# Optimization experiments

Hardware: AMD Instinct MI355X
Metric: run time of the kernel (lower is better)

## Reference

```python
import jax, jax.numpy as jnp
import numpy as np

B, N, DIM = 8, 1024, 768
HEADS, HEAD_DIM = 8, 96
EXPERTS, TASKS = 24, 9
SCALE = HEAD_DIM ** -0.5
SWITCHLOSS_W, ZLOSS_W = 0.1, 0.001


def setup_inputs() -> dict:
    key = jax.random.key(0)
    ks = jax.random.split(key, 6)
    x = jax.random.normal(ks[0], (B, N, DIM), jnp.float32)
    Wg = jax.random.normal(ks[1], (TASKS, DIM, EXPERTS), jnp.float32) * 0.02  # per-task gate
    W1 = jax.random.normal(ks[2], (EXPERTS, DIM, HEAD_DIM), jnp.float32) * 0.02  # experts (map)
    W2 = jax.random.normal(ks[3], (EXPERTS, HEAD_DIM, DIM), jnp.float32) * 0.02  # output_experts (reduce)
    Wkv = jax.random.normal(ks[4], (DIM, 2 * HEAD_DIM), jnp.float32) * 0.02      # shared kv proj
    b_kv = jax.random.normal(ks[5], (2 * HEAD_DIM,), jnp.float32) * 0.02
    return {"x": x, "Wg\u200b".replace("\u200b", ""): Wg, "W1": W1, "W2": W2, "Wkv": Wkv, "b_kv": b_kv, "task_bh": 3}


def reference(x, Wg, W1, W2, Wkv, b_kv, task_bh):
    # ---- TaskMoE top-k gating (eval mode: clean logits, no noise/sampling) ----
    logits = jnp.einsum('bnd,de->bne', x, Wg[task_bh])            # [B,N,E]
    probs = jax.nn.softmax(logits, axis=-1)
    top_g, top_i = jax.lax.top_k(probs, HEADS)                    # [B,N,H]
    denom = jax.lax.stop_gradient(jnp.sum(top_g, -1, keepdims=True) + 1e-6)
    gates = top_g / denom                                         # normalized top-k gates

    # ---- aux losses: switch (load-balance) + z-loss (cvloss weight is 0) ----
    me = probs.reshape(-1, EXPERTS).sum(0)
    me = me / me.sum()
    freqs = jnp.zeros((EXPERTS,), x.dtype).at[top_i.reshape(-1)].add(1.0)
    fe = freqs / freqs.sum()
    switch_loss = EXPERTS * jnp.sum(me * fe)
    z_loss = jnp.mean(jax.nn.logsumexp(logits.reshape(-1, EXPERTS), axis=-1) ** 2)
    aux_loss = SWITCHLOSS_W * switch_loss + ZLOSS_W * z_loss

    # ---- MoE map: per-head q from selected experts (dense compute + gather) ----
    all_q = jnp.einsum('bnd,edh->bneh', x, W1)                    # [B,N,E,Hd]
    q = jnp.take_along_axis(all_q, top_i[..., None], axis=2)      # [B,N,H,Hd]

    # ---- shared-KV multi-head attention ----
    kv = x @ Wkv + b_kv
    k, v = jnp.split(kv, 2, axis=-1)                              # [B,N,Hd] each
    attn = jnp.einsum('bihd,bjd->bhij', q, k) * SCALE             # [B,H,N,N]
    attn = jax.nn.softmax(attn, axis=-1)
    o = jnp.einsum('bhij,bjd->bihd', attn, v)                     # [B,N,H,Hd]

    # ---- MoE reduce: gate-weighted combine through output experts ----
    comb = jax.nn.one_hot(top_i, EXPERTS, dtype=x.dtype) * gates[..., None]  # [B,N,H,E]
    mixed = jnp.einsum('bnhe,bnhd->bned', comb, o)                # [B,N,E,Hd]
    out = jnp.einsum('bned,edc->bnc', mixed, W2)                  # [B,N,DIM]
    return out, aux_loss
```

## Files before the change

### kernel.cpp

```cpp
#include <hip/hip_runtime.h>
#include <hip/hip_bf16.h>
#include <stdint.h>

#define DEVFN static __device__ __forceinline__

typedef __attribute__((ext_vector_type(8))) short bf16x8;
typedef __attribute__((ext_vector_type(4))) short s16x4;
typedef __attribute__((ext_vector_type(4))) float f32x4;

static constexpr int TOK = 8192;
static constexpr int DIM = 768;
static constexpr int HEADS = 8;
static constexpr int HD = 96;
static constexpr int EXPERTS = 24;
static constexpr int NQ = 2304;
static constexpr int NQP = 2560;
static constexpr float C2 = 0.14724484f;
static constexpr float THRRAW = 78.0f;

static constexpr size_t OFF_XB   = 0;
static constexpr size_t OFF_BT1  = 12582912;
static constexpr size_t OFF_W2T  = 16515072;
static constexpr size_t OFF_K    = 20054016;
static constexpr size_t OFF_VT   = 21626880;
static constexpr size_t OFF_GATE = 23199744;
static constexpr size_t OFF_TOPI = 23461888;
static constexpr size_t OFF_AUX  = 23724032;
static constexpr size_t OFF_ALLQ = 23724288;
static constexpr size_t OFF_PART = OFF_ALLQ;
static constexpr size_t OFF_LOGT = OFF_ALLQ + 12582912;

DEVFN short f2bf(float f){
  __hip_bfloat16 h = __float2bfloat16(f);
  return __builtin_bit_cast(short, h);
}
DEVFN float bf2f(short u){
  return __bfloat162float(__builtin_bit_cast(__hip_bfloat16, u));
}

DEVFN void gload16(const void* g, void* l){
  auto gp = reinterpret_cast<__attribute__((address_space(1))) unsigned int*>(
      reinterpret_cast<uintptr_t>(g));
  auto lp = reinterpret_cast<__attribute__((address_space(3))) unsigned int*>(
      reinterpret_cast<uintptr_t>(l));
  __builtin_amdgcn_global_load_lds(gp, lp, 16, 0, 0);
}

__global__ __launch_bounds__(256) void prep_kernel(const float* __restrict__ W1,
                                                   const float* __restrict__ Wkv,
                                                   const float* __restrict__ W2,
                                                   short* __restrict__ Bt1,
                                                   short* __restrict__ W2t){
  __shared__ float tl[6240];
  int bid = blockIdx.x, tid = threadIdx.x;

  if (bid < 288){
    int e = bid / 12, dt = bid - e*12;
    int d0 = dt*64;
    const float* src = W1 + (size_t)e*(DIM*HD);
#pragma unroll
    for (int it = 0; it < 6; ++it){
      int c = it*256 + tid;
      int row = c / 24, q = c - row*24;
      float4 v = *reinterpret_cast<const float4*>(src + (size_t)(d0+row)*HD + q*4);
      float* dst = &tl[row*97 + q*4];
      dst[0]=v.x; dst[1]=v.y; dst[2]=v.z; dst[3]=v.w;
    }
    __syncthreads();
#pragma unroll
    for (int it = 0; it < 6; ++it){
      int c = it*256 + tid;
      int hh = c >> 4, cq = c & 15;
      s16x4 o4;
#pragma unroll
      for (int j = 0; j < 4; ++j) o4[j] = f2bf(tl[(cq*4+j)*97 + hh]);
      *reinterpret_cast<s16x4*>(Bt1 + (size_t)(e*HD + hh)*DIM + d0 + cq*4) = o4;
    }
  } else if (bid < 312){
    int t = bid - 288;
    int jb = t / 12, dt = t - jb*12;
    int j0 = jb*96, d0 = dt*64;
#pragma unroll
    for (int it = 0; it < 6; ++it){
      int c = it*256 + tid;
      int row = c / 24, q = c - row*24;
      float4 v = *reinterpret_cast<const float4*>(Wkv + (size_t)(d0+row)*192 + j0 + q*4);
      float* dst = &tl[row*97 + q*4];
      dst[0]=v.x; dst[1]=v.y; dst[2]=v.z; dst[3]=v.w;
    }
    __syncthreads();
#pragma unroll
    for (int it = 0; it < 6; ++it){
      int c = it*256 + tid;
      int jj = c >> 4, cq = c & 15;
      s16x4 o4;
#pragma unroll
      for (int j = 0; j < 4; ++j) o4[j] = f2bf(tl[(cq*4+j)*97 + jj]);
      *reinterpret_cast<s16x4*>(Bt1 + (size_t)(NQ + j0 + jj)*DIM + d0 + cq*4) = o4;
    }
  } else if (bid < 600){
    int t = bid - 312;
    int e = t / 12, ct = t - e*12;
    int c0 = ct*64;
    const float* src = W2 + (size_t)e*(HD*DIM);
#pragma unroll
    for (int it = 0; it < 6; ++it){
      int c = it*256 + tid;
      int hh = c >> 4, q = c & 15;
      float4 v = *reinterpret_cast<const float4*>(src + (size_t)hh*DIM + c0 + q*4);
      float* dst = &tl[hh*65 + q*4];
      dst[0]=v.x; dst[1]=v.y; dst[2]=v.z; dst[3]=v.w;
    }
    __syncthreads();
#pragma unroll
    for (int it = 0; it < 6; ++it){
      int c = it*256 + tid;
      int cr = c / 24, q = c - cr*24;
      s16x4 o4;
#pragma unroll
      for (int j = 0; j < 4; ++j) o4[j] = f2bf(tl[(q*4+j)*65 + cr]);
      *reinterpret_cast<s16x4*>(W2t + (size_t)(c0 + cr)*NQ + e*HD + q*4) = o4;
    }
  } else {
    int i = (bid-600)*256 + tid;
    Bt1[(size_t)(NQ + 192)*DIM + i] = 0;
  }
}

__global__ __launch_bounds__(64) void gating_partial(const float* __restrict__ x,
                                                     const float* __restrict__ Wg,
                                                     const int* __restrict__ task,
                                                     short* __restrict__ xb,
                                                     float* __restrict__ partial){
  __shared__ float xl[64*49];
  int lane = threadIdx.x;
  int tg = blockIdx.x >> 4, kc = blockIdx.x & 15;
  int tok0 = tg*64, kbase = kc*48;
  const float* Wt = Wg + (size_t)task[0]*(DIM*EXPERTS) + (size_t)kbase*EXPERTS;

#pragma unroll
  for (int i = 0; i < 12; ++i){
    int c = i*64 + lane;
    int t = c / 12, cc = c - t*12;
    size_t gidx = (size_t)(tok0+t)*DIM + kbase + cc*4;
    float4 v = *reinterpret_cast<const float4*>(x + gidx);
    float* dst = &xl[t*49 + cc*4];
    dst[0] = v.x; dst[1] = v.y; dst[2] = v.z; dst[3] = v.w;
    s16x4 o4;
    o4[0] = f2bf(v.x); o4[1] = f2bf(v.y); o4[2] = f2bf(v.z); o4[3] = f2bf(v.w);
    *reinterpret_cast<s16x4*>(xb + gidx) = o4;
  }
  __syncthreads();

  float acc[EXPERTS];
#pragma unroll
  for (int e = 0; e < EXPERTS; ++e) acc[e] = 0.f;
  for (int d = 0; d < 48; ++d){
    float xv = xl[lane*49 + d];
    const float* wr = Wt + d*EXPERTS;
#pragma unroll
    for (int e = 0; e < EXPERTS; ++e) acc[e] = fmaf(xv, wr[e], acc[e]);
  }
#pragma unroll
  for (int e = 0; e < EXPERTS; ++e)
    partial[(size_t)(kc*EXPERTS + e)*TOK + tok0 + lane] = acc[e];
}

__global__ __launch_bounds__(256) void gating_combine(const float* __restrict__ partial,
                                                      float* __restrict__ logT){
  int idx = blockIdx.x*256 + threadIdx.x;
  float s = 0.f;
#pragma unroll
  for (int kc = 0; kc < 16; ++kc)
    s += partial[(size_t)kc*EXPERTS*TOK + idx];
  logT[idx] = s;
}

__global__ __launch_bounds__(256) void gating_select(const float* __restrict__ logT,
                                                     int* __restrict__ topi,
                                                     float* __restrict__ gates,
                                                     float* __restrict__ auxbuf){
  __shared__ float lme[EXPERTS];
  __shared__ float lfr[EXPERTS];
  __shared__ float lz;
  int tid = threadIdx.x;
  int lane = tid & 63;
  int token = blockIdx.x*256 + tid;
  if (tid < EXPERTS){ lme[tid] = 0.f; lfr[tid] = 0.f; }
  if (tid == 0) lz = 0.f;
  __syncthreads();

  float acc[EXPERTS];
#pragma unroll
  for (int e = 0; e < EXPERTS; ++e)
    acc[e] = logT[(size_t)e*TOK + token];

  float mx = acc[0];
#pragma unroll
  for (int e = 1; e < EXPERTS; ++e) mx = fmaxf(mx, acc[e]);
  unsigned selm = 0; int sel[8]; float sg[8];
#pragma unroll
  for (int t = 0; t < 8; ++t){
    float best = -3.0e38f; int bi = 0;
#pragma unroll
    for (int e = 0; e < EXPERTS; ++e){
      bool ok = !((selm>>e)&1u) && (acc[e] > best);
      best = ok ? acc[e] : best;
      bi   = ok ? e      : bi;
    }
    selm |= (1u<<bi); sel[t] = bi; sg[t] = best;
  }

  float p[EXPERTS]; float S = 0.f;
#pragma unroll
  for (int e = 0; e < EXPERTS; ++e){ p[e] = __expf(acc[e] - mx); S += p[e]; }
  float lse = mx + __logf(S);
  float Sinv = 1.f/S;
  float gsum = 0.f; float pg[8];
#pragma unroll
  for (int t = 0; t < 8; ++t){ pg[t] = __expf(sg[t] - mx)*Sinv; gsum += pg[t]; }
  float dinv = 1.f/(gsum + 1e-6f);

#pragma unroll
  for (int t = 0; t < 8; ++t){
    topi[token*HEADS + t]  = sel[t];
    gates[token*HEADS + t] = pg[t]*dinv;
  }

  float z2 = lse*lse;
#pragma unroll
  for (int d = 1; d < 64; d <<= 1) z2 += __shfl_xor(z2, d, 64);
#pragma unroll
  for (int e = 0; e < EXPERTS; ++e){
    float v = p[e]*Sinv;
#pragma unroll
    for (int d = 1; d < 64; d <<= 1) v += __shfl_xor(v, d, 64);
    bool hit = (sel[0]==e)|(sel[1]==e)|(sel[2]==e)|(sel[3]==e)|
               (sel[4]==e)|(sel[5]==e)|(sel[6]==e)|(sel[7]==e);
    unsigned long long bal = __ballot(hit);
    if (lane == 0){
      atomicAdd(&lme[e], v);
      atomicAdd(&lfr[e], (float)__popcll(bal));
    }
  }
  if (lane == 0) atomicAdd(&lz, z2);
  __syncthreads();
  if (tid < EXPERTS){
    atomicAdd(&auxbuf[tid], lme[tid]);
    atomicAdd(&auxbuf[EXPERTS + tid], lfr[tid]);
  } else if (tid == 63) atomicAdd(&auxbuf[2*EXPERTS], lz);
}

__global__ void aux_final(const float* __restrict__ auxbuf, float* __restrict__ outa){
  if (threadIdx.x != 0 || blockIdx.x != 0) return;
  float ms = 0.f, fs = 0.f;
  for (int e=0;e<EXPERTS;++e){ ms += auxbuf[e]; fs += auxbuf[EXPERTS+e]; }
  float sw = 0.f;
  for (int e=0;e<EXPERTS;++e) sw += (auxbuf[e]/ms)*(auxbuf[EXPERTS+e]/fs);
  sw *= (float)EXPERTS;
  float z = auxbuf[2*EXPERTS] / (float)TOK;
  outa[0] = 0.1f*sw + 0.001f*z;
}

template<bool OUT_BF16>
__global__ __launch_bounds__(256) void gemm_bt(const short* __restrict__ A,
                                               const short* __restrict__ Bt,
                                               void* __restrict__ Cout,
                                               int M, int N, int K){
  __shared__ short As[128*64];
  __shared__ short Bs[128*64];
  int nwg = gridDim.x*gridDim.y;
  int orig = blockIdx.y*gridDim.x + blockIdx.x;
  int cpx = nwg >> 3;
  int swz = (orig & 7)*cpx + (orig >> 3);
  int bx = swz % gridDim.x, by = swz / gridDim.x;

  int tid = threadIdx.x;
  int lane = tid & 63, w = tid >> 6;
  int wr = w >> 1, wc = w & 1;
  int l15 = lane & 15, lg = lane >> 4;
  int m0 = by * 128, n0 = bx * 128;

  f32x4 acc[4][4] = {};

  for (int k0 = 0; k0 < K; k0 += 64){
#pragma unroll
    for (int it = 0; it < 4; ++it){
      int c = it*256 + tid;
      int row = c >> 3, cc = c & 7;
      int csrc = cc ^ (row & 7);
      gload16(A  + (size_t)(m0+row)*K + k0 + csrc*8, (char*)As + (size_t)c*16);
      gload16(Bt + (size_t)(n0+row)*K + k0 + csrc*8, (char*)Bs + (size_t)c*16);
    }
    __syncthreads();
#pragma unroll
    for (int kk = 0; kk < 2; ++kk){
      bf16x8 af[4], bfr[4];
      int jp = (kk*4 + lg) ^ (l15 & 7);
#pragma unroll
      for (int m = 0; m < 4; ++m)
        af[m] = *reinterpret_cast<const bf16x8*>(&As[(wr*64 + m*16 + l15)*64 + jp*8]);
#pragma unroll
      for (int n = 0; n < 4; ++n)
        bfr[n] = *reinterpret_cast<const bf16x8*>(&Bs[(wc*64 + n*16 + l15)*64 + jp*8]);
#pragma unroll
      for (int m = 0; m < 4; ++m)
#pragma unroll
        for (int n = 0; n < 4; ++n)
          acc[m][n] = __builtin_amdgcn_mfma_f32_16x16x32_bf16(af[m], bfr[n], acc[m][n], 0, 0, 0);
    }
    __syncthreads();
  }
#pragma unroll
  for (int m = 0; m < 4; ++m)
#pragma unroll
    for (int n = 0; n < 4; ++n){
      int rbase = m0 + wr*64 + m*16 + lg*4;
      int col   = n0 + wc*64 + n*16 + l15;
#pragma unroll
      for (int r = 0; r < 4; ++r){
        float v = acc[m][n][r];
        size_t idx = (size_t)(rbase + r)*N + col;
        if constexpr (OUT_BF16) ((short*)Cout)[idx] = f2bf(v);
        else                    ((float*)Cout)[idx] = v;
      }
    }
}

__global__ __launch_bounds__(256) void gemm2_fused(const short* __restrict__ o,
                                                   const int* __restrict__ topi,
                                                   const short* __restrict__ W2t,
                                                   float* __restrict__ out){
  __shared__ short As[2][128*64];
  __shared__ short Bs[2][64*64];
  __shared__ signed char hmap[128][24];
  int nwg = gridDim.x*gridDim.y;
  int orig = blockIdx.y*gridDim.x + blockIdx.x;
  int cpx = nwg >> 3;
  int swz = (orig & 7)*cpx + (orig >> 3);
  int bx = swz % gridDim.x, by = swz / gridDim.x;

  int tid = threadIdx.x;
  int lane = tid & 63, w = tid >> 6;
  int l15 = lane & 15, lg = lane >> 4;
  int m0 = by * 128, n0 = bx * 64;

  int* hm32 = (int*)&hmap[0][0];
  for (int i = tid; i < 768; i += 256) hm32[i] = -1;
  __syncthreads();
  for (int i = tid; i < 128*8; i += 256){
    int row = i >> 3, hh = i & 7;
    int e = topi[(size_t)(m0+row)*HEADS + hh];
    hmap[row][e] = (signed char)hh;
  }
  __syncthreads();

  int arow[4], accv[4];
  size_t arbase[4];
#pragma unroll
  for (int it = 0; it < 4; ++it){
    int c = it*256 + tid;
    arow[it] = c >> 3; accv[it] = c & 7;
    arbase[it] = (size_t)(m0 + arow[it])*DIM;
  }

  f32x4 acc[2][4] = {};
  bf16x8 areg[4];

#define STAGE_A(kt, dst)                                                     \
  {                                                                          \
    _Pragma("unroll")                                                        \
    for (int it = 0; it < 4; ++it){                                          \
      unsigned kc = (unsigned)((kt)*8 + accv[it]);                           \
      unsigned e = kc / 12u;                                                 \
      unsigned dc = kc - e*12u;                                              \
      int hh = hmap[arow[it]][e];                                            \
      bf16x8 av = {};                                                        \
      if (hh >= 0)                                                           \
        av = *reinterpret_cast<const bf16x8*>(o + arbase[it] + hh*HD + dc*8);\
      dst[it] = av;                                                          \
    }                                                                        \
  }
#define WRITE_A(buf, src)                                                    \
  {                                                                          \
    _Pragma("unroll")                                                        \
    for (int it = 0; it < 4; ++it)                                           \
      *reinterpret_cast<bf16x8*>(                                            \
        &As[buf][arow[it]*64 + ((accv[it] ^ (arow[it] & 7)))*8]) = src[it];  \
  }
#define STAGE_B(kt, buf)                                                     \
  {                                                                          \
    _Pragma("unroll")                                                        \
    for (int it = 0; it < 2; ++it){                                          \
      int c = it*256 + tid;                                                  \
      int row = c >> 3, cc = c & 7;                                          \
      int csrc = cc ^ (row & 7);                                             \
      gload16(W2t + (size_t)(n0+row)*NQ + (kt)*64 + csrc*8,                  \
              (char*)&Bs[buf][0] + (size_t)c*16);                            \
    }                                                                        \
  }

  STAGE_A(0, areg);
  STAGE_B(0, 0);
  WRITE_A(0, areg);
  __syncthreads();

  for (int kt = 0; kt < 36; ++kt){
    int buf = kt & 1;
    bf16x8 anext[4];
    if (kt < 35){
      STAGE_A(kt+1, anext);
      STAGE_B(kt+1, buf^1);
    }
#pragma unroll
    for (int kk = 0; kk < 2; ++kk){
      int jp = (kk*4 + lg) ^ (l15 & 7);
      bf16x8 af[2], bfr[4];
#pragma unroll
      for (int m = 0; m < 2; ++m)
        af[m] = *reinterpret_cast<const bf16x8*>(&As[buf][(w*32 + m*16 + l15)*64 + jp*8]);
#pragma unroll
      for (int n = 0; n < 4; ++n)
        bfr[n] = *reinterpret_cast<const bf16x8*>(&Bs[buf][(n*16 + l15)*64 + jp*8]);
#pragma unroll
      for (int m = 0; m < 2; ++m)
#pragma unroll
        for (int n = 0; n < 4; ++n)
          acc[m][n] = __builtin_amdgcn_mfma_f32_16x16x32_bf16(af[m], bfr[n], acc[m][n], 0, 0, 0);
    }
    if (kt < 35) WRITE_A(buf^1, anext);
    __syncthreads();
  }
#undef STAGE_A
#undef WRITE_A
#undef STAGE_B

#pragma unroll
  for (int m = 0; m < 2; ++m)
#pragma unroll
    for (int n = 0; n < 4; ++n){
      int rbase = m0 + w*32 + m*16 + lg*4;
      int col   = n0 + n*16 + l15;
#pragma unroll
      for (int r = 0; r < 4; ++r)
        out[(size_t)(rbase + r)*DIM + col] = acc[m][n][r];
    }
}

__global__ __launch_bounds__(256) void split_kv_tile(const short* __restrict__ allq,
                                                     const float* __restrict__ bkv,
                                                     short* __restrict__ Kp,
                                                     short* __restrict__ Vp){
  __shared__ short kv[64*192];
  int bt = blockIdx.x;
  int b = bt >> 4;
  int tid = threadIdx.x;
#pragma unroll
  for (int it = 0; it < 6; ++it){
    int c = it*256 + tid;
    int j = c / 24, cc = c - j*24;
    int token = b*1024 + (bt & 15)*64 + j;
    gload16(allq + (size_t)token*NQP + NQ + cc*8, (char*)kv + (size_t)c*16);
  }
  __syncthreads();
#pragma unroll
  for (int it = 0; it < 3; ++it){
    int c = it*256 + tid;
    int kc = c >> 6, j = c & 63;
    bf16x8 v = *reinterpret_cast<const bf16x8*>(&kv[j*192 + kc*8]);
    bf16x8 o8;
#pragma unroll
    for (int e = 0; e < 8; ++e) o8[e] = f2bf(bf2f(v[e]) + bkv[kc*8 + e]);
    *reinterpret_cast<bf16x8*>(Kp + ((size_t)bt*768 + c)*8) = o8;
  }
#pragma unroll
  for (int it = 0; it < 3; ++it){
    int c = it*256 + tid;
    int kc = c / 96, hd = c - kc*96;
    float bias = bkv[96 + hd];
    bf16x8 o8;
#pragma unroll
    for (int e = 0; e < 8; ++e) o8[e] = f2bf(bf2f(kv[(kc*8 + e)*192 + 96 + hd]) + bias);
    *reinterpret_cast<bf16x8*>(Vp + ((size_t)bt*768 + c)*8) = o8;
  }
}

__global__ __launch_bounds__(256, 2) void attn_fwd(const short* __restrict__ allq,
                                                   const int* __restrict__ topi,
                                                   const float* __restrict__ gates,
                                                   const short* __restrict__ Kp,
                                                   const short* __restrict__ Vp,
                                                   short* __restrict__ o){
  __shared__ short Klds[2][768*8];
  __shared__ short Vlds[2][768*8];
  __shared__ short Plds[4][16*72];
  int qt = blockIdx.x, bh = blockIdx.y;
  int b = bh >> 3, h = bh & 7;
  int tid = threadIdx.x;
  int lane = tid & 63, w = tid >> 6;
  int l15 = lane & 15, lg = lane >> 4;

  bf16x8 qf[2][3];
  int tok0 = b*1024 + qt*128 + w*32;
#pragma unroll
  for (int qm = 0; qm < 2; ++qm){
    int token = tok0 + qm*16 + l15;
    int qe = topi[token*HEADS + h];
    const short* qp = allq + (size_t)token*NQP + qe*HD;
#pragma unroll
    for (int t = 0; t < 3; ++t)
      qf[qm][t] = *reinterpret_cast<const bf16x8*>(qp + t*32 + lg*8);
  }

  f32x4 Oacc[2][6] = {};
  float mrun[2][4], lrun[2][4];
#pragma unroll
  for (int qm = 0; qm < 2; ++qm)
#pragma unroll
    for (int r = 0; r < 4; ++r){ mrun[qm][r] = -1.0e30f; lrun[qm][r] = 0.f; }

  const short* kb = Kp + (size_t)b*16*768*8;
  const short* vb = Vp + (size_t)b*16*768*8;

#pragma unroll
  for (int it = 0; it < 3; ++it){
    int c = it*256 + tid;
    gload16(kb + (size_t)c*8, (char*)&Klds[0][0] + (size_t)c*16);
    gload16(vb + (size_t)c*8, (char*)&Vlds[0][0] + (size_t)c*16);
  }
  __syncthreads();

  int cur = 0;
  for (int nt = 0; nt < 16; ++nt){
    if (nt < 15){
      const short* kn = kb + (size_t)(nt+1)*768*8;
      const short* vn = vb + (size_t)(nt+1)*768*8;
#pragma unroll
      for (int it = 0; it < 3; ++it){
        int c = it*256 + tid;
        gload16(kn + (size_t)c*8, (char*)&Klds[cur^1][0] + (size_t)c*16);
        gload16(vn + (size_t)c*8, (char*)&Vlds[cur^1][0] + (size_t)c*16);
      }
    }

    f32x4 sa[2][4];
    __builtin_amdgcn_s_setprio(1);
#pragma unroll
    for (int ct = 0; ct < 4; ++ct){
      bf16x8 kf[3];
#pragma unroll
      for (int t = 0; t < 3; ++t)
        kf[t] = *reinterpret_cast<const bf16x8*>(&Klds[cur][((t*4+lg)*64 + ct*16 + l15)*8]);
#pragma unroll
      for (int qm = 0; qm < 2; ++qm){
        f32x4 a = {};
#pragma unroll
        for (int t = 0; t < 3; ++t)
          a = __builtin_amdgcn_mfma_f32_16x16x32_bf16(qf[qm][t], kf[t], a, 0, 0, 0);
        sa[qm][ct] = a;
      }
    }
    __builtin_amdgcn_s_setprio(0);

    float pmax[2][4];
    bool need = false;
#pragma unroll
    for (int qm = 0; qm < 2; ++qm)
#pragma unroll
      for (int r = 0; r < 4; ++r){
        pmax[qm][r] = fmaxf(fmaxf(sa[qm][0][r], sa[qm][1][r]),
                            fmaxf(sa[qm][2][r], sa[qm][3][r]));
        need = need || (pmax[qm][r] > mrun[qm][r] + THRRAW);
      }
    if (__any(need)){
#pragma unroll
      for (int qm = 0; qm < 2; ++qm)
#pragma unroll
        for (int r = 0; r < 4; ++r){
          float mx = pmax[qm][r];
#pragma unroll
          for (int d = 1; d < 16; d <<= 1) mx = fmaxf(mx, __shfl_xor(mx, d, 64));
          float mnew = fmaxf(mrun[qm][r], mx);
          float al = exp2f((mrun[qm][r] - mnew)*C2);
          lrun[qm][r] *= al;
#pragma unroll
          for (int dt = 0; dt < 6; ++dt) Oacc[qm][dt][r] *= al;
          mrun[qm][r] = mnew;
        }
    }

#pragma unroll
    for (int qm = 0; qm < 2; ++qm)
#pragma unroll
      for (int r = 0; r < 4; ++r){
        float mc = mrun[qm][r]*C2;
        float s = 0.f;
#pragma unroll
        for (int ct = 0; ct < 4; ++ct){
          float p = exp2f(fmaf(sa[qm][ct][r], C2, -mc));
          sa[qm][ct][r] = p; s += p;
        }
        lrun[qm][r] += s;
      }

    bf16x8 vf[2][6];
#pragma unroll
    for (int ct = 0; ct < 4; ++ct)
#pragma unroll
      for (int r = 0; r < 4; ++r)
        Plds[w][(lg*4 + r)*72 + ct*16 + l15] = f2bf(sa[0][ct][r]);
    __builtin_amdgcn_s_setprio(1);
#pragma unroll
    for (int ks = 0; ks < 2; ++ks){
      bf16x8 pa = *reinterpret_cast<const bf16x8*>(&Plds[w][l15*72 + ks*32 + lg*8]);
#pragma unroll
      for (int dt = 0; dt < 6; ++dt){
        vf[ks][dt] = *reinterpret_cast<const bf16x8*>(&Vlds[cur][((ks*4+lg)*96 + dt*16 + l15)*8]);
        Oacc[0][dt] = __builtin_amdgcn_mfma_f32_16x16x32_bf16(pa, vf[ks][dt], Oacc[0][dt], 0, 0, 0);
      }
    }
    __builtin_amdgcn_s_setprio(0);
#pragma unroll
    for (int ct = 0; ct < 4; ++ct)
#pragma unroll
      for (int r = 0; r < 4; ++r)
        Plds[w][(lg*4 + r)*72 + ct*16 + l15] = f2bf(sa[1][ct][r]);
    __builtin_amdgcn_s_setprio(1);
#pragma unroll
    for (int ks = 0; ks < 2; ++ks){
      bf16x8 pa = *reinterpret_cast<const bf16x8*>(&Plds[w][l15*72 + ks*32 + lg*8]);
#pragma unroll
      for (int dt = 0; dt < 6; ++dt)
        Oacc[1][dt] = __builtin_amdgcn_mfma_f32_16x16x32_bf16(pa, vf[ks][dt], Oacc[1][dt], 0, 0, 0);
    }
    __builtin_amdgcn_s_setprio(0);

    __syncthreads();
    cur ^= 1;
  }

#pragma unroll
  for (int qm = 0; qm < 2; ++qm)
#pragma unroll
    for (int r = 0; r < 4; ++r){
      float l = lrun[qm][r];
#pragma unroll
      for (int d = 1; d < 16; d <<= 1) l += __shfl_xor(l, d, 64);
      int token = tok0 + qm*16 + lg*4 + r;
      float inv = gates[token*HEADS + h] / l;
#pragma unroll
      for (int dt = 0; dt < 6; ++dt)
        o[(size_t)token*DIM + h*HD + dt*16 + l15] = f2bf(Oacc[qm][dt][r]*inv);
    }
}

extern "C" void kernel_launch(void* const* d_in, const int* in_sizes, int n_in,
                              void* d_out, int out_size, void* d_ws, size_t ws_size,
                              hipStream_t stream) {
  (void)in_sizes; (void)n_in; (void)out_size; (void)ws_size;
  const float* x    = (const float*)d_in[0];
  const float* Wg   = (const float*)d_in[1];
  const float* W1   = (const float*)d_in[2];
  const float* W2   = (const float*)d_in[3];
  const float* Wkv  = (const float*)d_in[4];
  const float* bkv  = (const float*)d_in[5];
  const int*   task = (const int*)d_in[6];

  char* ws = (char*)d_ws;
  short* xb    = (short*)(ws + OFF_XB);
  short* o     = (short*)(ws + OFF_XB);
  short* Bt1   = (short*)(ws + OFF_BT1);
  short* W2t   = (short*)(ws + OFF_W2T);
  short* Kp    = (short*)(ws + OFF_K);
  short* Vp    = (short*)(ws + OFF_VT);
  float* gates = (float*)(ws + OFF_GATE);
  int*   topi  = (int*)(ws + OFF_TOPI);
  float* aux   = (float*)(ws + OFF_AUX);
  short* allq  = (short*)(ws + OFF_ALLQ);
  float* part  = (float*)(ws + OFF_PART);
  float* logT  = (float*)(ws + OFF_LOGT);
  float* out   = (float*)d_out;

  hipMemsetAsync(aux, 0, 256, stream);
  prep_kernel   <<<792, 256, 0, stream>>>(W1, Wkv, W2, Bt1, W2t);
  gating_partial<<<2048, 64, 0, stream>>>(x, Wg, task, xb, part);
  gating_combine<<<768, 256, 0, stream>>>(part, logT);
  gating_select <<<32, 256, 0, stream>>>(logT, topi, gates, aux);
  aux_final     <<<1, 64, 0, stream>>>(aux, out + (size_t)TOK*DIM);
  gemm_bt<true><<<dim3(NQP/128, TOK/128), 256, 0, stream>>>(xb, Bt1, allq, TOK, NQP, DIM);
  split_kv_tile<<<128, 256, 0, stream>>>(allq, bkv, Kp, Vp);
  attn_fwd     <<<dim3(8, 64), 256, 0, stream>>>(allq, topi, gates, Kp, Vp, o);
  gemm2_fused  <<<dim3(DIM/64, TOK/128), 256, 0, stream>>>(o, topi, W2t, out);
}
```

Measured before the change: 187.6 us.

## Shrink attention tiles and interleave K/V per 32-key block for higher occupancy

The attention kernel now gives each wave 16 query rows instead of 32 and walks the keys in 32-key steps instead of 64. K and V for each step are packed into one contiguous 12 KB block, so each step is a single combined prefetch. The smaller register and LDS footprint allows four blocks per CU and twice as many blocks. The cost is that K/V data is reloaded from global memory twice as often per query, and the loop runs more iterations with a barrier on each.

Result: slower. 192.4 us (+2.6%).

```diff
diff --git a/kernel.cpp b/kernel.cpp
--- a/kernel.cpp
+++ b/kernel.cpp
@@ -22,7 +22,6 @@
 static constexpr size_t OFF_BT1  = 12582912;
 static constexpr size_t OFF_W2T  = 16515072;
 static constexpr size_t OFF_K    = 20054016;
-static constexpr size_t OFF_VT   = 21626880;
 static constexpr size_t OFF_GATE = 23199744;
 static constexpr size_t OFF_TOPI = 23461888;
 static constexpr size_t OFF_AUX  = 23724032;
@@ -449,8 +448,7 @@
 
 __global__ __launch_bounds__(256) void split_kv_tile(const short* __restrict__ allq,
                                                      const float* __restrict__ bkv,
-                                                     short* __restrict__ Kp,
-                                                     short* __restrict__ Vp){
+                                                     short* __restrict__ KVp){
   __shared__ short kv[64*192];
   int bt = blockIdx.x;
   int b = bt >> 4;
@@ -466,172 +464,137 @@
 #pragma unroll
   for (int it = 0; it < 3; ++it){
     int c = it*256 + tid;
-    int kc = c >> 6, j = c & 63;
-    bf16x8 v = *reinterpret_cast<const bf16x8*>(&kv[j*192 + kc*8]);
+    int h = c / 384, r = c - h*384;
+    int kc = r >> 5, j = r & 31;
+    bf16x8 v = *reinterpret_cast<const bf16x8*>(&kv[(h*32 + j)*192 + kc*8]);
     bf16x8 o8;
 #pragma unroll
     for (int e = 0; e < 8; ++e) o8[e] = f2bf(bf2f(v[e]) + bkv[kc*8 + e]);
-    *reinterpret_cast<bf16x8*>(Kp + ((size_t)bt*768 + c)*8) = o8;
+    *reinterpret_cast<bf16x8*>(KVp + ((size_t)(bt*2 + h)*6144) + (size_t)(kc*32 + j)*8) = o8;
   }
 #pragma unroll
   for (int it = 0; it < 3; ++it){
     int c = it*256 + tid;
-    int kc = c / 96, hd = c - kc*96;
+    int h = c / 384, r = c - h*384;
+    int kc = r / 96, hd = r - kc*96;
     float bias = bkv[96 + hd];
     bf16x8 o8;
 #pragma unroll
-    for (int e = 0; e < 8; ++e) o8[e] = f2bf(bf2f(kv[(kc*8 + e)*192 + 96 + hd]) + bias);
-    *reinterpret_cast<bf16x8*>(Vp + ((size_t)bt*768 + c)*8) = o8;
-  }
-}
-
-__global__ __launch_bounds__(256, 2) void attn_fwd(const short* __restrict__ allq,
+    for (int e = 0; e < 8; ++e)
+      o8[e] = f2bf(bf2f(kv[(h*32 + kc*8 + e)*192 + 96 + hd]) + bias);
+    *reinterpret_cast<bf16x8*>(KVp + ((size_t)(bt*2 + h)*6144) + 3072 + (size_t)(kc*96 + hd)*8) = o8;
+  }
+}
+
+__global__ __launch_bounds__(256, 4) void attn_fwd(const short* __restrict__ allq,
                                                    const int* __restrict__ topi,
                                                    const float* __restrict__ gates,
-                                                   const short* __restrict__ Kp,
-                                                   const short* __restrict__ Vp,
+                                                   const short* __restrict__ KVp,
                                                    short* __restrict__ o){
-  __shared__ short Klds[2][768*8];
-  __shared__ short Vlds[2][768*8];
-  __shared__ short Plds[4][16*72];
+  __shared__ short KV[2][6144];
+  __shared__ short Plds[4][640];
   int qt = blockIdx.x, bh = blockIdx.y;
   int b = bh >> 3, h = bh & 7;
   int tid = threadIdx.x;
   int lane = tid & 63, w = tid >> 6;
   int l15 = lane & 15, lg = lane >> 4;
 
-  bf16x8 qf[2][3];
-  int tok0 = b*1024 + qt*128 + w*32;
-#pragma unroll
-  for (int qm = 0; qm < 2; ++qm){
-    int token = tok0 + qm*16 + l15;
-    int qe = topi[token*HEADS + h];
-    const short* qp = allq + (size_t)token*NQP + qe*HD;
-#pragma unroll
-    for (int t = 0; t < 3; ++t)
-      qf[qm][t] = *reinterpret_cast<const bf16x8*>(qp + t*32 + lg*8);
-  }
-
-  f32x4 Oacc[2][6] = {};
-  float mrun[2][4], lrun[2][4];
-#pragma unroll
-  for (int qm = 0; qm < 2; ++qm)
-#pragma unroll
-    for (int r = 0; r < 4; ++r){ mrun[qm][r] = -1.0e30f; lrun[qm][r] = 0.f; }
-
-  const short* kb = Kp + (size_t)b*16*768*8;
-  const short* vb = Vp + (size_t)b*16*768*8;
+  int tok0 = b*1024 + qt*64 + w*16;
+  int token0 = tok0 + l15;
+  int qe = topi[token0*HEADS + h];
+  const short* qp = allq + (size_t)token0*NQP + qe*HD;
+  bf16x8 qf[3];
+#pragma unroll
+  for (int t = 0; t < 3; ++t)
+    qf[t] = *reinterpret_cast<const bf16x8*>(qp + t*32 + lg*8);
+
+  f32x4 Oacc[6] = {};
+  float mrun[4], lrun[4];
+#pragma unroll
+  for (int r = 0; r < 4; ++r){ mrun[r] = -1.0e30f; lrun[r] = 0.f; }
+
+  const short* kvb = KVp + (size_t)b*32*6144;
 
 #pragma unroll
   for (int it = 0; it < 3; ++it){
     int c = it*256 + tid;
-    gload16(kb + (size_t)c*8, (char*)&Klds[0][0] + (size_t)c*16);
-    gload16(vb + (size_t)c*8, (char*)&Vlds[0][0] + (size_t)c*16);
+    gload16(kvb + (size_t)c*8, (char*)&KV[0][0] + (size_t)c*16);
   }
   __syncthreads();
 
   int cur = 0;
-  for (int nt = 0; nt < 16; ++nt){
-    if (nt < 15){
-      const short* kn = kb + (size_t)(nt+1)*768*8;
-      const short* vn = vb + (size_t)(nt+1)*768*8;
+  for (int nt = 0; nt < 32; ++nt){
+    if (nt < 31){
+      const short* kn = kvb + (size_t)(nt+1)*6144;
 #pragma unroll
       for (int it = 0; it < 3; ++it){
         int c = it*256 + tid;
-        gload16(kn + (size_t)c*8, (char*)&Klds[cur^1][0] + (size_t)c*16);
-        gload16(vn + (size_t)c*8, (char*)&Vlds[cur^1][0] + (size_t)c*16);
+        gload16(kn + (size_t)c*8, (char*)&KV[cur^1][0] + (size_t)c*16);
       }
     }
 
-    f32x4 sa[2][4];
+    f32x4 sa[2];
     __builtin_amdgcn_s_setprio(1);
 #pragma unroll
-    for (int ct = 0; ct < 4; ++ct){
-      bf16x8 kf[3];
-#pragma unroll
-      for (int t = 0; t < 3; ++t)
-        kf[t] = *reinterpret_cast<const bf16x8*>(&Klds[cur][((t*4+lg)*64 + ct*16 + l15)*8]);
-#pragma unroll
-      for (int qm = 0; qm < 2; ++qm){
-        f32x4 a = {};
-#pragma unroll
-        for (int t = 0; t < 3; ++t)
-          a = __builtin_amdgcn_mfma_f32_16x16x32_bf16(qf[qm][t], kf[t], a, 0, 0, 0);
-        sa[qm][ct] = a;
+    for (int ct = 0; ct < 2; ++ct){
+      f32x4 a = {};
+#pragma unroll
+      for (int t = 0; t < 3; ++t){
+        bf16x8 kf = *reinterpret_cast<const bf16x8*>(&KV[cur][((t*4+lg)*32 + ct*16 + l15)*8]);
+        a = __builtin_amdgcn_mfma_f32_16x16x32_bf16(qf[t], kf, a, 0, 0, 0);
       }
+      sa[ct] = a;
     }
     __builtin_amdgcn_s_setprio(0);
 
-    float pmax[2][4];
+    float pmax[4];
     bool need = false;
 #pragma unroll
-    for (int qm = 0; qm < 2; ++qm)
+    for (int r = 0; r < 4; ++r){
+      pmax[r] = fmaxf(sa[0][r], sa[1][r]);
+      need = need || (pmax[r] > mrun[r] + THRRAW);
+    }
+    if (__any(need)){
 #pragma unroll
       for (int r = 0; r < 4; ++r){
-        pmax[qm][r] = fmaxf(fmaxf(sa[qm][0][r], sa[qm][1][r]),
-                            fmaxf(sa[qm][2][r], sa[qm][3][r]));
-        need = need || (pmax[qm][r] > mrun[qm][r] + THRRAW);
+        float mx = pmax[r];
+#pragma unroll
+        for (int d = 1; d < 16; d <<= 1) mx = fmaxf(mx, __shfl_xor(mx, d, 64));
+        float mnew = fmaxf(mrun[r], mx);
+        float al = exp2f((mrun[r] - mnew)*C2);
+        lrun[r] *= al;
+#pragma unroll
+        for (int dt = 0; dt < 6; ++dt) Oacc[dt][r] *= al;
+        mrun[r] = mnew;
       }
-    if (__any(need)){
-#pragma unroll
-      for (int qm = 0; qm < 2; ++qm)
-#pragma unroll
-        for (int r = 0; r < 4; ++r){
-          float mx = pmax[qm][r];
-#pragma unroll
-          for (int d = 1; d < 16; d <<= 1) mx = fmaxf(mx, __shfl_xor(mx, d, 64));
-          float mnew = fmaxf(mrun[qm][r], mx);
-          float al = exp2f((mrun[qm][r] - mnew)*C2);
-          lrun[qm][r] *= al;
-#pragma unroll
-          for (int dt = 0; dt < 6; ++dt) Oacc[qm][dt][r] *= al;
-          mrun[qm][r] = mnew;
-        }
-    }
-
-#pragma unroll
-    for (int qm = 0; qm < 2; ++qm)
-#pragma unroll
-      for (int r = 0; r < 4; ++r){
-        float mc = mrun[qm][r]*C2;
-        float s = 0.f;
-#pragma unroll
-        for (int ct = 0; ct < 4; ++ct){
-          float p = exp2f(fmaf(sa[qm][ct][r], C2, -mc));
-          sa[qm][ct][r] = p; s += p;
-        }
-        lrun[qm][r] += s;
+    }
+
+#pragma unroll
+    for (int r = 0; r < 4; ++r){
+      float mc = mrun[r]*C2;
+      float s = 0.f;
+#pragma unroll
+      for (int ct = 0; ct < 2; ++ct){
+        float p = exp2f(fmaf(sa[ct][r], C2, -mc));
+        sa[ct][r] = p; s += p;
       }
-
-    bf16x8 vf[2][6];
-#pragma unroll
-    for (int ct = 0; ct < 4; ++ct)
+      lrun[r] += s;
+    }
+
+#pragma unroll
+    for (int ct = 0; ct < 2; ++ct)
 #pragma unroll
       for (int r = 0; r < 4; ++r)
-        Plds[w][(lg*4 + r)*72 + ct*16 + l15] = f2bf(sa[0][ct][r]);
+        Plds[w][(lg*4 + r)*40 + ct*16 + l15] = f2bf(sa[ct][r]);
+
     __builtin_amdgcn_s_setprio(1);
-#pragma unroll
-    for (int ks = 0; ks < 2; ++ks){
-      bf16x8 pa = *reinterpret_cast<const bf16x8*>(&Plds[w][l15*72 + ks*32 + lg*8]);
+    {
+      bf16x8 pa = *reinterpret_cast<const bf16x8*>(&Plds[w][l15*40 + lg*8]);
 #pragma unroll
       for (int dt = 0; dt < 6; ++dt){
-        vf[ks][dt] = *reinterpret_cast<const bf16x8*>(&Vlds[cur][((ks*4+lg)*96 + dt*16 + l15)*8]);
-        Oacc[0][dt] = __builtin_amdgcn_mfma_f32_16x16x32_bf16(pa, vf[ks][dt], Oacc[0][dt], 0, 0, 0);
+        bf16x8 vf = *reinterpret_cast<const bf16x8*>(&KV[cur][3072 + ((lg*96) + dt*16 + l15)*8]);
+        Oacc[dt] = __builtin_amdgcn_mfma_f32_16x16x32_bf16(pa, vf, Oacc[dt], 0, 0, 0);
       }
-    }
-    __builtin_amdgcn_s_setprio(0);
-#pragma unroll
-    for (int ct = 0; ct < 4; ++ct)
-#pragma unroll
-      for (int r = 0; r < 4; ++r)
-        Plds[w][(lg*4 + r)*72 + ct*16 + l15] = f2bf(sa[1][ct][r]);
-    __builtin_amdgcn_s_setprio(1);
-#pragma unroll
-    for (int ks = 0; ks < 2; ++ks){
-      bf16x8 pa = *reinterpret_cast<const bf16x8*>(&Plds[w][l15*72 + ks*32 + lg*8]);
-#pragma unroll
-      for (int dt = 0; dt < 6; ++dt)
-        Oacc[1][dt] = __builtin_amdgcn_mfma_f32_16x16x32_bf16(pa, vf[ks][dt], Oacc[1][dt], 0, 0, 0);
     }
     __builtin_amdgcn_s_setprio(0);
 
@@ -640,18 +603,16 @@
   }
 
 #pragma unroll
-  for (int qm = 0; qm < 2; ++qm)
-#pragma unroll
-    for (int r = 0; r < 4; ++r){
-      float l = lrun[qm][r];
-#pragma unroll
-      for (int d = 1; d < 16; d <<= 1) l += __shfl_xor(l, d, 64);
-      int token = tok0 + qm*16 + lg*4 + r;
-      float inv = gates[token*HEADS + h] / l;
-#pragma unroll
-      for (int dt = 0; dt < 6; ++dt)
-        o[(size_t)token*DIM + h*HD + dt*16 + l15] = f2bf(Oacc[qm][dt][r]*inv);
-    }
+  for (int r = 0; r < 4; ++r){
+    float l = lrun[r];
+#pragma unroll
+    for (int d = 1; d < 16; d <<= 1) l += __shfl_xor(l, d, 64);
+    int token = tok0 + lg*4 + r;
+    float inv = gates[token*HEADS + h] / l;
+#pragma unroll
+    for (int dt = 0; dt < 6; ++dt)
+      o[(size_t)token*DIM + h*HD + dt*16 + l15] = f2bf(Oacc[dt][r]*inv);
+  }
 }
 
 extern "C" void kernel_launch(void* const* d_in, const int* in_sizes, int n_in,
@@ -671,8 +632,7 @@
   short* o     = (short*)(ws + OFF_XB);
   short* Bt1   = (short*)(ws + OFF_BT1);
   short* W2t   = (short*)(ws + OFF_W2T);
-  short* Kp    = (short*)(ws + OFF_K);
-  short* Vp    = (short*)(ws + OFF_VT);
+  short* KVp   = (short*)(ws + OFF_K);
   float* gates = (float*)(ws + OFF_GATE);
   int*   topi  = (int*)(ws + OFF_TOPI);
   float* aux   = (float*)(ws + OFF_AUX);
@@ -688,7 +648,7 @@
   gating_select <<<32, 256, 0, stream>>>(logT, topi, gates, aux);
   aux_final     <<<1, 64, 0, stream>>>(aux, out + (size_t)TOK*DIM);
   gemm_bt<true><<<dim3(NQP/128, TOK/128), 256, 0, stream>>>(xb, Bt1, allq, TOK, NQP, DIM);
-  split_kv_tile<<<128, 256, 0, stream>>>(allq, bkv, Kp, Vp);
-  attn_fwd     <<<dim3(8, 64), 256, 0, stream>>>(allq, topi, gates, Kp, Vp, o);
+  split_kv_tile<<<128, 256, 0, stream>>>(allq, bkv, KVp);
+  attn_fwd     <<<dim3(16, 64), 256, 0, stream>>>(allq, topi, gates, KVp, o);
   gemm2_fused  <<<dim3(DIM/64, TOK/128), 256, 0, stream>>>(o, topi, W2t, out);
 }
```
